# Optimization experiments

Measured on AMD Instinct MI355X. Metric: run time of the kernel, lower is better.

The kernel has to match this reference:

```python
import jax, jax.numpy as jnp
import numpy as np

N_NODES = 100000
N_EDGES = 3200000
IN_FEAT = 512
HID = 32
N_CLASSES = 10


def gcn_conv(x, W, b, src, dst, num_nodes):
    """PyG GCNConv: linear transform, then symmetric-normalized aggregation
    with self-loops. out_i = sum_{j->i} norm_ij * (x_j W) + d_i^{-1} * (x_i W) + b."""
    h = x @ W  # [N, out]
    ones = jnp.ones(src.shape[0], dtype=x.dtype)
    deg = jax.ops.segment_sum(ones, dst, num_segments=num_nodes) + 1.0  # +1 self-loop
    dinv = jax.lax.rsqrt(deg)
    norm = dinv[src] * dinv[dst]  # [E]
    msg = h[src] * norm[:, None]  # [E, out]
    agg = jax.ops.segment_sum(msg, dst, num_segments=num_nodes)
    agg = agg + h * (dinv * dinv)[:, None]  # self-loop term (norm = d^-1)
    return agg + b


def setup_inputs() -> dict:
    key = jax.random.key(0)
    ks = jax.random.split(key, 12)
    x0 = jax.random.normal(ks[0], (N_NODES, IN_FEAT), dtype=jnp.float32)
    edge_index = jax.random.randint(ks[1], (2, N_EDGES), 0, N_NODES, dtype=jnp.int64)
    batch = jnp.zeros((N_NODES,), dtype=jnp.int64)

    def glorot(k, shape):
        fan_in, fan_out = shape
        lim = jnp.sqrt(6.0 / (fan_in + fan_out)).astype(jnp.float32)
        return jax.random.uniform(k, shape, jnp.float32, -lim, lim)

    return {
        "x0": x0,
        "edge_index": edge_index,
        "batch": batch,
        "W1": glorot(ks[2], (IN_FEAT, HID)),
        "b1": jnp.zeros((HID,), jnp.float32),
        "W2": glorot(ks[3], (HID, HID)),
        "b2": jnp.zeros((HID,), jnp.float32),
        "W3": glorot(ks[4], (HID, HID)),
        "b3": jnp.zeros((HID,), jnp.float32),
        "lin1_W": glorot(ks[5], (HID, 16)),
        "lin1_b": jnp.zeros((16,), jnp.float32),
        "lin2_W": glorot(ks[6], (16, N_CLASSES)),
        "lin2_b": jnp.zeros((N_CLASSES,), jnp.float32),
    }


def reference(x0, edge_index, batch, W1, b1, W2, b2, W3, b3,
              lin1_W, lin1_b, lin2_W, lin2_b):
    src, dst = edge_index[0], edge_index[1]
    n = x0.shape[0]
    x1 = jax.nn.relu(gcn_conv(x0, W1, b1, src, dst, n))
    x2 = jax.nn.relu(gcn_conv(x1, W2, b2, src, dst, n))
    x3 = jax.nn.relu(gcn_conv(x2, W3, b3, src, dst, n))
    # NOTE: original code computes cat([x1,x2,x3]) but then uses only x3; we match that.
    x = jax.nn.relu(x3 @ lin1_W + lin1_b)
    # dropout p=0.5 is identity in eval mode
    x = x @ lin2_W + lin2_b
    return x
```

## Files before the change

kernel.cpp:

```cpp
#include <hip/hip_runtime.h>
#include <hip/hip_bf16.h>

typedef float f32x4 __attribute__((ext_vector_type(4)));

#define N_NODES 100000
#define NCHUNK 16

__global__ void k_detect(const int* __restrict__ ei, int* __restrict__ mode) {
    __shared__ int flag;
    if (threadIdx.x == 0) flag = 0;
    __syncthreads();
    int f = 0;
    for (int i = threadIdx.x; i < 4096; i += 256)
        if (ei[2 * i + 1] != 0) f = 1;
    if (f) flag = 1;
    __syncthreads();
    if (threadIdx.x == 0) *mode = flag;
}

__global__ void k_zero(int* p, int n) {
    int i = blockIdx.x * 256 + threadIdx.x;
    if (i < n) p[i] = 0;
}

__global__ void k_pack_hist(const int* __restrict__ ei, const int* __restrict__ mode,
                            int2* __restrict__ pairs, int* __restrict__ cnt, int E) {
    int e = blockIdx.x * 256 + threadIdx.x;
    if (e >= E) return;
    int m = *mode;
    int s = m ? ei[e] : ei[2 * e];
    int d = m ? ei[E + e] : ei[2 * (E + e)];
    if ((unsigned)s >= N_NODES) s = 0;
    if ((unsigned)d >= N_NODES) d = 0;
    int2 p; p.x = s; p.y = d;
    pairs[e] = p;
    atomicAdd(&cnt[d], 1);
}

__global__ void k_bsum(const int* __restrict__ cnt, int* __restrict__ bsum, int n) {
    __shared__ int s[256];
    int tid = threadIdx.x;
    int i = blockIdx.x * 256 + tid;
    s[tid] = (i < n) ? cnt[i] : 0;
    __syncthreads();
    for (int d = 128; d > 0; d >>= 1) {
        if (tid < d) s[tid] += s[tid + d];
        __syncthreads();
    }
    if (tid == 0) bsum[blockIdx.x] = s[0];
}

__global__ void k_scan_top(const int* __restrict__ bsum, int* __restrict__ boff, int nb) {
    __shared__ int s[512];
    int tid = threadIdx.x;
    int v = (tid < nb) ? bsum[tid] : 0;
    s[tid] = v;
    __syncthreads();
    for (int d = 1; d < 512; d <<= 1) {
        int t = (tid >= d) ? s[tid - d] : 0;
        __syncthreads();
        s[tid] += t;
        __syncthreads();
    }
    if (tid < nb) boff[tid] = s[tid] - v;
}

__global__ void k_scan_bot(const int* __restrict__ cnt, const int* __restrict__ boff,
                           int* __restrict__ rowptr, float* __restrict__ dinv,
                           int* __restrict__ fill, int n) {
    __shared__ int s[256];
    int tid = threadIdx.x;
    int i = blockIdx.x * 256 + tid;
    int v = (i < n) ? cnt[i] : 0;
    s[tid] = v;
    __syncthreads();
    for (int d = 1; d < 256; d <<= 1) {
        int t = (tid >= d) ? s[tid - d] : 0;
        __syncthreads();
        s[tid] += t;
        __syncthreads();
    }
    int incl = s[tid];
    if (i < n) {
        rowptr[i] = boff[blockIdx.x] + incl - v;
        if (i == n - 1) rowptr[n] = boff[blockIdx.x] + incl;
        dinv[i] = rsqrtf((float)v + 1.0f);
        fill[i] = 0;
    }
}

__global__ __launch_bounds__(256) void k_scatter(const int4* __restrict__ pairs4,
                                                 const int* __restrict__ rowptr,
                                                 int* __restrict__ fill,
                                                 int* __restrict__ csr, int half) {
    int gtid = blockIdx.x * 256 + threadIdx.x;
    int gstride = gridDim.x * 256;
    const int CH = (N_NODES + NCHUNK - 1) / NCHUNK;
    for (int c = 0; c < NCHUNK; c++) {
        int lo = c * CH;
        for (int i = gtid; i < half; i += gstride) {
            int4 p = pairs4[i];
            if ((unsigned)(p.y - lo) < (unsigned)CH) {
                int pos = rowptr[p.y] + atomicAdd(&fill[p.y], 1);
                csr[pos] = p.x;
            }
            if ((unsigned)(p.w - lo) < (unsigned)CH) {
                int pos = rowptr[p.w] + atomicAdd(&fill[p.w], 1);
                csr[pos] = p.z;
            }
        }
    }
}

__global__ __launch_bounds__(256) void k_gemm1(const float* __restrict__ X,
                                               const float* __restrict__ W,
                                               float* __restrict__ H) {
    __shared__ float lds[8448];
    float* xs  = lds;
    float* wsw = lds + 4160;
    int tid = threadIdx.x;
    int row = tid & 63;
    int kc  = tid >> 6;
    long row0 = (long)blockIdx.x * 64;

    float acc[32];
#pragma unroll
    for (int c = 0; c < 32; c++) acc[c] = 0.f;

    for (int k0 = 0; k0 < 512; k0 += 64) {
        __syncthreads();
#pragma unroll
        for (int u = 0; u < 8; u++) {
            int idx = u * 256 + tid;
            wsw[idx] = W[k0 * 32 + idx];
        }
#pragma unroll
        for (int u = 0; u < 4; u++) {
            int idx = u * 256 + tid;
            int rr = idx >> 4, j = idx & 15;
            long grow = row0 + rr;
            f32x4 v = {0.f, 0.f, 0.f, 0.f};
            if (grow < N_NODES) v = *(const f32x4*)&X[grow * 512 + k0 + 4 * j];
            float* dp = &xs[rr * 65 + 4 * j];
            dp[0] = v.x; dp[1] = v.y; dp[2] = v.z; dp[3] = v.w;
        }
        __syncthreads();
        int kbase = kc * 16;
#pragma unroll
        for (int kk = 0; kk < 16; kk++) {
            float xk = xs[row * 65 + kbase + kk];
            const float* wrow = &wsw[(kbase + kk) * 32];
#pragma unroll
            for (int c = 0; c < 32; c += 4) {
                f32x4 wv = *(const f32x4*)&wrow[c];
                acc[c]     += xk * wv.x;
                acc[c + 1] += xk * wv.y;
                acc[c + 2] += xk * wv.z;
                acc[c + 3] += xk * wv.w;
            }
        }
    }
    __syncthreads();
#pragma unroll
    for (int c = 0; c < 32; c++) lds[(kc * 64 + row) * 33 + c] = acc[c];
    __syncthreads();
#pragma unroll
    for (int i = 0; i < 8; i++) {
        int o = i * 256 + tid;
        int r = o >> 5, c = o & 31;
        float s = lds[r * 33 + c] + lds[(64 + r) * 33 + c]
                + lds[(128 + r) * 33 + c] + lds[(192 + r) * 33 + c];
        long grow = row0 + r;
        if (grow < N_NODES) H[grow * 32 + c] = s;
    }
}

__global__ __launch_bounds__(256) void k_agg_mm(const float* __restrict__ H,
                                                const int* __restrict__ rowptr,
                                                const int* __restrict__ csr,
                                                const float* __restrict__ dinv,
                                                const float* __restrict__ bias,
                                                const float* __restrict__ W,
                                                float* __restrict__ Hout, int n) {
    __shared__ float ws[1024];
    int tid = threadIdx.x;
    for (int t = tid; t < 1024; t += 256) ws[t] = W[t];
    __syncthreads();
    int node = blockIdx.x * 8 + (tid >> 5);
    int f = tid & 31;
    if (node >= n) return;
    int e0 = rowptr[node], e1 = rowptr[node + 1];
    float a0 = 0.f, a1 = 0.f, a2 = 0.f, a3 = 0.f;
    int e = e0;
    for (; e + 3 < e1; e += 4) {
        int s0 = csr[e], s1 = csr[e + 1], s2 = csr[e + 2], s3 = csr[e + 3];
        a0 += H[(long)s0 * 32 + f] * dinv[s0];
        a1 += H[(long)s1 * 32 + f] * dinv[s1];
        a2 += H[(long)s2 * 32 + f] * dinv[s2];
        a3 += H[(long)s3 * 32 + f] * dinv[s3];
    }
    for (; e < e1; e++) {
        int s0 = csr[e];
        a0 += H[(long)s0 * 32 + f] * dinv[s0];
    }
    float dv = dinv[node];
    float v = ((a0 + a1) + (a2 + a3)) * dv + H[(long)node * 32 + f] * dv * dv + bias[f];
    v = fmaxf(v, 0.f);
    float o = 0.f;
#pragma unroll
    for (int k = 0; k < 32; k++) {
        float vk = __shfl(v, k, 32);
        o += vk * ws[k * 32 + f];
    }
    Hout[(long)node * 32 + f] = o;
}

__global__ __launch_bounds__(256) void k_agg_head(const float* __restrict__ H,
                                                  const int* __restrict__ rowptr,
                                                  const int* __restrict__ csr,
                                                  const float* __restrict__ dinv,
                                                  const float* __restrict__ bias,
                                                  const float* __restrict__ L1W,
                                                  const float* __restrict__ L1B,
                                                  const float* __restrict__ L2W,
                                                  const float* __restrict__ L2B,
                                                  float* __restrict__ out, int n) {
    __shared__ float w1[512];
    __shared__ float w2[160];
    __shared__ float bb1[16];
    __shared__ float bb2[10];
    int tid = threadIdx.x;
    for (int t = tid; t < 512; t += 256) w1[t] = L1W[t];
    if (tid < 160) w2[tid] = L2W[tid];
    if (tid < 16) bb1[tid] = L1B[tid];
    if (tid < 10) bb2[tid] = L2B[tid];
    __syncthreads();
    int node = blockIdx.x * 8 + (tid >> 5);
    int f = tid & 31;
    if (node >= n) return;
    int e0 = rowptr[node], e1 = rowptr[node + 1];
    float a0 = 0.f, a1 = 0.f, a2 = 0.f, a3 = 0.f;
    int e = e0;
    for (; e + 3 < e1; e += 4) {
        int s0 = csr[e], s1 = csr[e + 1], s2 = csr[e + 2], s3 = csr[e + 3];
        a0 += H[(long)s0 * 32 + f] * dinv[s0];
        a1 += H[(long)s1 * 32 + f] * dinv[s1];
        a2 += H[(long)s2 * 32 + f] * dinv[s2];
        a3 += H[(long)s3 * 32 + f] * dinv[s3];
    }
    for (; e < e1; e++) {
        int s0 = csr[e];
        a0 += H[(long)s0 * 32 + f] * dinv[s0];
    }
    float dv = dinv[node];
    float v = ((a0 + a1) + (a2 + a3)) * dv + H[(long)node * 32 + f] * dv * dv + bias[f];
    v = fmaxf(v, 0.f);
    int c1 = f & 15;
    float t1 = 0.f;
#pragma unroll
    for (int k = 0; k < 32; k++) {
        float vk = __shfl(v, k, 32);
        t1 += vk * w1[k * 16 + c1];
    }
    t1 = fmaxf(t1 + bb1[c1], 0.f);
    int c2 = (f < 10) ? f : 0;
    float o = 0.f;
#pragma unroll
    for (int k = 0; k < 16; k++) {
        float tk = __shfl(t1, k, 32);
        o += tk * w2[k * 10 + c2];
    }
    o += bb2[c2];
    if (f < 10) out[(long)node * 10 + f] = o;
}

extern "C" void kernel_launch(void* const* d_in, const int* in_sizes, int n_in,
                              void* d_out, int out_size, void* d_ws, size_t ws_size,
                              hipStream_t stream) {
    const float* x0 = (const float*)d_in[0];
    const int* ei = (const int*)d_in[1];
    const float* W1 = (const float*)d_in[3];
    const float* b1 = (const float*)d_in[4];
    const float* W2 = (const float*)d_in[5];
    const float* b2 = (const float*)d_in[6];
    const float* W3 = (const float*)d_in[7];
    const float* b3 = (const float*)d_in[8];
    const float* l1W = (const float*)d_in[9];
    const float* l1b = (const float*)d_in[10];
    const float* l2W = (const float*)d_in[11];
    const float* l2b = (const float*)d_in[12];

    const int E = in_sizes[1] / 2;
    const int N = N_NODES;

    char* w = (char*)d_ws;
    float* h      = (float*)(w);
    float* xb     = (float*)(w + 12800000);
    int2*  pairs  = (int2*) (w);
    int*   cnt    = (int*)  (w + 25600000);
    int*   rowptr = (int*)  (w + 26000000);
    float* dinv   = (float*)(w + 26400016);
    int*   fill   = (int*)  (w + 26800016);
    int*   bsum   = (int*)  (w + 27200016);
    int*   boff   = (int*)  (w + 27204016);
    int*   csr    = (int*)  (w + 27208016);
    int*   mode   = (int*)  (w + 40008016);

    const int NB  = (N + 255) / 256;
    const int EB  = (E + 255) / 256;
    const int AGB = (N + 7) / 8;
    const int G1B = (N + 63) / 64;

    k_detect<<<1, 256, 0, stream>>>(ei, mode);
    k_zero<<<NB, 256, 0, stream>>>(cnt, N);
    k_pack_hist<<<EB, 256, 0, stream>>>(ei, mode, pairs, cnt, E);
    k_bsum<<<NB, 256, 0, stream>>>(cnt, bsum, N);
    k_scan_top<<<1, 512, 0, stream>>>(bsum, boff, NB);
    k_scan_bot<<<NB, 256, 0, stream>>>(cnt, boff, rowptr, dinv, fill, N);
    k_scatter<<<1024, 256, 0, stream>>>((const int4*)pairs, rowptr, fill, csr, E / 2);

    k_gemm1<<<G1B, 256, 0, stream>>>(x0, W1, h);
    k_agg_mm<<<AGB, 256, 0, stream>>>(h, rowptr, csr, dinv, b1, W2, xb, N);
    k_agg_mm<<<AGB, 256, 0, stream>>>(xb, rowptr, csr, dinv, b2, W3, h, N);
    k_agg_head<<<AGB, 256, 0, stream>>>(h, rowptr, csr, dinv, b3,
                                        l1W, l1b, l2W, l2b, (float*)d_out, N);
}
```

Measured before the change: 924.3 us.

## Build CSR via two-level bucket sort and pre-scale features by dinv

Replaces the global-atomic histogram and the chunked 16-pass scatter with a two-level counting sort. Per-block LDS histograms over 256-node buckets feed column scans, edges are bucketized, then each bucket builds its CSR slice with LDS atomics. Source features are pre-multiplied by dinv in the GEMM and aggregation epilogues, which removes the per-edge dinv gather. The gather loop now loads 32 neighbor indices cooperatively and broadcasts them with shuffles. In exchange it adds more kernel launches and an intermediate bucketed pair buffer, and it reorders the floating-point summation.

```diff
diff --git a/kernel.cpp b/kernel.cpp
--- a/kernel.cpp
+++ b/kernel.cpp
@@ -4,7 +4,9 @@
 typedef float f32x4 __attribute__((ext_vector_type(4)));
 
 #define N_NODES 100000
-#define NCHUNK 16
+#define NBUK 391
+#define BSHIFT 8
+#define HBLK 256
 
 __global__ void k_detect(const int* __restrict__ ei, int* __restrict__ mode) {
     __shared__ int flag;
@@ -18,42 +20,41 @@
     if (threadIdx.x == 0) *mode = flag;
 }
 
-__global__ void k_zero(int* p, int n) {
-    int i = blockIdx.x * 256 + threadIdx.x;
-    if (i < n) p[i] = 0;
-}
-
-__global__ void k_pack_hist(const int* __restrict__ ei, const int* __restrict__ mode,
-                            int2* __restrict__ pairs, int* __restrict__ cnt, int E) {
-    int e = blockIdx.x * 256 + threadIdx.x;
-    if (e >= E) return;
+__global__ __launch_bounds__(256) void k_hist(const int* __restrict__ ei,
+                                              const int* __restrict__ mode,
+                                              int* __restrict__ gh, int E, int chunk) {
+    __shared__ int hist[NBUK];
+    int tid = threadIdx.x, k = blockIdx.x;
+    for (int b = tid; b < NBUK; b += 256) hist[b] = 0;
+    __syncthreads();
     int m = *mode;
-    int s = m ? ei[e] : ei[2 * e];
-    int d = m ? ei[E + e] : ei[2 * (E + e)];
-    if ((unsigned)s >= N_NODES) s = 0;
-    if ((unsigned)d >= N_NODES) d = 0;
-    int2 p; p.x = s; p.y = d;
-    pairs[e] = p;
-    atomicAdd(&cnt[d], 1);
-}
-
-__global__ void k_bsum(const int* __restrict__ cnt, int* __restrict__ bsum, int n) {
+    int e0 = k * chunk, e1 = min(E, e0 + chunk);
+    for (int e = e0 + tid; e < e1; e += 256) {
+        int d = m ? ei[E + e] : ei[2 * (E + e)];
+        if ((unsigned)d >= N_NODES) d = 0;
+        atomicAdd(&hist[d >> BSHIFT], 1);
+    }
+    __syncthreads();
+    for (int b = tid; b < NBUK; b += 256) gh[k * NBUK + b] = hist[b];
+}
+
+__global__ __launch_bounds__(256) void k_btot(const int* __restrict__ gh, int* __restrict__ btot) {
     __shared__ int s[256];
-    int tid = threadIdx.x;
-    int i = blockIdx.x * 256 + tid;
-    s[tid] = (i < n) ? cnt[i] : 0;
+    int b = blockIdx.x, tid = threadIdx.x;
+    s[tid] = gh[tid * NBUK + b];
     __syncthreads();
     for (int d = 128; d > 0; d >>= 1) {
         if (tid < d) s[tid] += s[tid + d];
         __syncthreads();
     }
-    if (tid == 0) bsum[blockIdx.x] = s[0];
-}
-
-__global__ void k_scan_top(const int* __restrict__ bsum, int* __restrict__ boff, int nb) {
+    if (tid == 0) btot[b] = s[0];
+}
+
+__global__ void k_scan_btot(const int* __restrict__ btot, int* __restrict__ bbase,
+                            int* __restrict__ rowptr, int E) {
     __shared__ int s[512];
     int tid = threadIdx.x;
-    int v = (tid < nb) ? bsum[tid] : 0;
+    int v = (tid < NBUK) ? btot[tid] : 0;
     s[tid] = v;
     __syncthreads();
     for (int d = 1; d < 512; d <<= 1) {
@@ -62,16 +63,14 @@
         s[tid] += t;
         __syncthreads();
     }
-    if (tid < nb) boff[tid] = s[tid] - v;
-}
-
-__global__ void k_scan_bot(const int* __restrict__ cnt, const int* __restrict__ boff,
-                           int* __restrict__ rowptr, float* __restrict__ dinv,
-                           int* __restrict__ fill, int n) {
+    if (tid < NBUK) bbase[tid] = s[tid] - v;
+    if (tid == 0) { bbase[NBUK] = E; rowptr[N_NODES] = E; }
+}
+
+__global__ __launch_bounds__(256) void k_scan_cols(int* __restrict__ gh, const int* __restrict__ bbase) {
     __shared__ int s[256];
-    int tid = threadIdx.x;
-    int i = blockIdx.x * 256 + tid;
-    int v = (i < n) ? cnt[i] : 0;
+    int b = blockIdx.x, tid = threadIdx.x;
+    int v = gh[tid * NBUK + b];
     s[tid] = v;
     __syncthreads();
     for (int d = 1; d < 256; d <<= 1) {
@@ -80,40 +79,76 @@
         s[tid] += t;
         __syncthreads();
     }
-    int incl = s[tid];
-    if (i < n) {
-        rowptr[i] = boff[blockIdx.x] + incl - v;
-        if (i == n - 1) rowptr[n] = boff[blockIdx.x] + incl;
-        dinv[i] = rsqrtf((float)v + 1.0f);
-        fill[i] = 0;
-    }
-}
-
-__global__ __launch_bounds__(256) void k_scatter(const int4* __restrict__ pairs4,
-                                                 const int* __restrict__ rowptr,
-                                                 int* __restrict__ fill,
-                                                 int* __restrict__ csr, int half) {
-    int gtid = blockIdx.x * 256 + threadIdx.x;
-    int gstride = gridDim.x * 256;
-    const int CH = (N_NODES + NCHUNK - 1) / NCHUNK;
-    for (int c = 0; c < NCHUNK; c++) {
-        int lo = c * CH;
-        for (int i = gtid; i < half; i += gstride) {
-            int4 p = pairs4[i];
-            if ((unsigned)(p.y - lo) < (unsigned)CH) {
-                int pos = rowptr[p.y] + atomicAdd(&fill[p.y], 1);
-                csr[pos] = p.x;
-            }
-            if ((unsigned)(p.w - lo) < (unsigned)CH) {
-                int pos = rowptr[p.w] + atomicAdd(&fill[p.w], 1);
-                csr[pos] = p.z;
-            }
-        }
+    gh[tid * NBUK + b] = bbase[b] + s[tid] - v;
+}
+
+__global__ __launch_bounds__(256) void k_bucketize(const int* __restrict__ ei,
+                                                   const int* __restrict__ mode,
+                                                   const int* __restrict__ offs,
+                                                   int2* __restrict__ bp, int E, int chunk) {
+    __shared__ int cur[NBUK];
+    int tid = threadIdx.x, k = blockIdx.x;
+    for (int b = tid; b < NBUK; b += 256) cur[b] = offs[k * NBUK + b];
+    __syncthreads();
+    int m = *mode;
+    int e0 = k * chunk, e1 = min(E, e0 + chunk);
+    for (int e = e0 + tid; e < e1; e += 256) {
+        int s, d;
+        if (m) { s = ei[e]; d = ei[E + e]; }
+        else   { s = ei[2 * e]; d = ei[2 * (E + e)]; }
+        if ((unsigned)s >= N_NODES) s = 0;
+        if ((unsigned)d >= N_NODES) d = 0;
+        int pos = atomicAdd(&cur[d >> BSHIFT], 1);
+        int2 p; p.x = s; p.y = d;
+        bp[pos] = p;
+    }
+}
+
+__global__ __launch_bounds__(256) void k_build_csr(const int2* __restrict__ bp,
+                                                   const int* __restrict__ bbase,
+                                                   int* __restrict__ rowptr,
+                                                   float* __restrict__ dinv,
+                                                   int* __restrict__ csr) {
+    __shared__ int cnt[256];
+    __shared__ int s[256];
+    __shared__ int cur[256];
+    int b = blockIdx.x, tid = threadIdx.x;
+    int nb = b << BSHIFT;
+    int estart = bbase[b], eend = bbase[b + 1];
+    cnt[tid] = 0;
+    __syncthreads();
+    for (int e = estart + tid; e < eend; e += 256) {
+        int2 p = bp[e];
+        atomicAdd(&cnt[p.y - nb], 1);
+    }
+    __syncthreads();
+    int v = cnt[tid];
+    s[tid] = v;
+    __syncthreads();
+    for (int d = 1; d < 256; d <<= 1) {
+        int t = (tid >= d) ? s[tid - d] : 0;
+        __syncthreads();
+        s[tid] += t;
+        __syncthreads();
+    }
+    int excl = s[tid] - v;
+    int node = nb + tid;
+    if (node < N_NODES) {
+        rowptr[node] = estart + excl;
+        dinv[node] = rsqrtf((float)v + 1.0f);
+    }
+    cur[tid] = estart + excl;
+    __syncthreads();
+    for (int e = estart + tid; e < eend; e += 256) {
+        int2 p = bp[e];
+        int pos = atomicAdd(&cur[p.y - nb], 1);
+        csr[pos] = p.x;
     }
 }
 
 __global__ __launch_bounds__(256) void k_gemm1(const float* __restrict__ X,
                                                const float* __restrict__ W,
+                                               const float* __restrict__ dinv,
                                                float* __restrict__ H) {
     __shared__ float lds[8448];
     float* xs  = lds;
@@ -168,11 +203,41 @@
     for (int i = 0; i < 8; i++) {
         int o = i * 256 + tid;
         int r = o >> 5, c = o & 31;
-        float s = lds[r * 33 + c] + lds[(64 + r) * 33 + c]
-                + lds[(128 + r) * 33 + c] + lds[(192 + r) * 33 + c];
+        float sv = lds[r * 33 + c] + lds[(64 + r) * 33 + c]
+                 + lds[(128 + r) * 33 + c] + lds[(192 + r) * 33 + c];
         long grow = row0 + r;
-        if (grow < N_NODES) H[grow * 32 + c] = s;
-    }
+        if (grow < N_NODES) H[grow * 32 + c] = sv * dinv[grow];
+    }
+}
+
+__device__ __forceinline__ float gather_sum(const float* __restrict__ Hf,
+                                            const int* __restrict__ csr,
+                                            int e0, int e1, int f) {
+    float a0 = 0.f, a1 = 0.f, a2 = 0.f, a3 = 0.f;
+    for (int base = e0; base < e1; base += 32) {
+        int idx = base + f;
+        int sl = (idx < e1) ? csr[idx] : 0;
+        int mm = e1 - base;
+        if (mm >= 32) {
+#pragma unroll
+            for (int j = 0; j < 32; j += 4) {
+                int s0 = __shfl(sl, j, 32);
+                int s1 = __shfl(sl, j + 1, 32);
+                int s2 = __shfl(sl, j + 2, 32);
+                int s3 = __shfl(sl, j + 3, 32);
+                a0 += Hf[(long)s0 * 32];
+                a1 += Hf[(long)s1 * 32];
+                a2 += Hf[(long)s2 * 32];
+                a3 += Hf[(long)s3 * 32];
+            }
+        } else {
+            for (int j = 0; j < mm; j++) {
+                int s0 = __shfl(sl, j, 32);
+                a0 += Hf[(long)s0 * 32];
+            }
+        }
+    }
+    return (a0 + a1) + (a2 + a3);
 }
 
 __global__ __launch_bounds__(256) void k_agg_mm(const float* __restrict__ H,
@@ -190,21 +255,10 @@
     int f = tid & 31;
     if (node >= n) return;
     int e0 = rowptr[node], e1 = rowptr[node + 1];
-    float a0 = 0.f, a1 = 0.f, a2 = 0.f, a3 = 0.f;
-    int e = e0;
-    for (; e + 3 < e1; e += 4) {
-        int s0 = csr[e], s1 = csr[e + 1], s2 = csr[e + 2], s3 = csr[e + 3];
-        a0 += H[(long)s0 * 32 + f] * dinv[s0];
-        a1 += H[(long)s1 * 32 + f] * dinv[s1];
-        a2 += H[(long)s2 * 32 + f] * dinv[s2];
-        a3 += H[(long)s3 * 32 + f] * dinv[s3];
-    }
-    for (; e < e1; e++) {
-        int s0 = csr[e];
-        a0 += H[(long)s0 * 32 + f] * dinv[s0];
-    }
+    const float* Hf = H + f;
+    float asum = gather_sum(Hf, csr, e0, e1, f);
     float dv = dinv[node];
-    float v = ((a0 + a1) + (a2 + a3)) * dv + H[(long)node * 32 + f] * dv * dv + bias[f];
+    float v = dv * (asum + Hf[(long)node * 32]) + bias[f];
     v = fmaxf(v, 0.f);
     float o = 0.f;
 #pragma unroll
@@ -212,7 +266,7 @@
         float vk = __shfl(v, k, 32);
         o += vk * ws[k * 32 + f];
     }
-    Hout[(long)node * 32 + f] = o;
+    Hout[(long)node * 32 + f] = o * dv;
 }
 
 __global__ __launch_bounds__(256) void k_agg_head(const float* __restrict__ H,
@@ -239,21 +293,10 @@
     int f = tid & 31;
     if (node >= n) return;
     int e0 = rowptr[node], e1 = rowptr[node + 1];
-    float a0 = 0.f, a1 = 0.f, a2 = 0.f, a3 = 0.f;
-    int e = e0;
-    for (; e + 3 < e1; e += 4) {
-        int s0 = csr[e], s1 = csr[e + 1], s2 = csr[e + 2], s3 = csr[e + 3];
-        a0 += H[(long)s0 * 32 + f] * dinv[s0];
-        a1 += H[(long)s1 * 32 + f] * dinv[s1];
-        a2 += H[(long)s2 * 32 + f] * dinv[s2];
-        a3 += H[(long)s3 * 32 + f] * dinv[s3];
-    }
-    for (; e < e1; e++) {
-        int s0 = csr[e];
-        a0 += H[(long)s0 * 32 + f] * dinv[s0];
-    }
+    const float* Hf = H + f;
+    float asum = gather_sum(Hf, csr, e0, e1, f);
     float dv = dinv[node];
-    float v = ((a0 + a1) + (a2 + a3)) * dv + H[(long)node * 32 + f] * dv * dv + bias[f];
+    float v = dv * (asum + Hf[(long)node * 32]) + bias[f];
     v = fmaxf(v, 0.f);
     int c1 = f & 15;
     float t1 = 0.f;
@@ -296,30 +339,28 @@
     char* w = (char*)d_ws;
     float* h      = (float*)(w);
     float* xb     = (float*)(w + 12800000);
-    int2*  pairs  = (int2*) (w);
-    int*   cnt    = (int*)  (w + 25600000);
-    int*   rowptr = (int*)  (w + 26000000);
-    float* dinv   = (float*)(w + 26400016);
-    int*   fill   = (int*)  (w + 26800016);
-    int*   bsum   = (int*)  (w + 27200016);
-    int*   boff   = (int*)  (w + 27204016);
-    int*   csr    = (int*)  (w + 27208016);
-    int*   mode   = (int*)  (w + 40008016);
-
-    const int NB  = (N + 255) / 256;
-    const int EB  = (E + 255) / 256;
+    int2*  bp     = (int2*) (w);
+    int*   gh     = (int*)  (w + 25600000);
+    int*   btot   = (int*)  (w + 26000384);
+    int*   bbase  = (int*)  (w + 26001948);
+    int*   rowptr = (int*)  (w + 26003516);
+    float* dinv   = (float*)(w + 26403532);
+    int*   csr    = (int*)  (w + 26803532);
+    int*   mode   = (int*)  (w + 39603532);
+
+    const int chunk = (E + HBLK - 1) / HBLK;
     const int AGB = (N + 7) / 8;
     const int G1B = (N + 63) / 64;
 
     k_detect<<<1, 256, 0, stream>>>(ei, mode);
-    k_zero<<<NB, 256, 0, stream>>>(cnt, N);
-    k_pack_hist<<<EB, 256, 0, stream>>>(ei, mode, pairs, cnt, E);
-    k_bsum<<<NB, 256, 0, stream>>>(cnt, bsum, N);
-    k_scan_top<<<1, 512, 0, stream>>>(bsum, boff, NB);
-    k_scan_bot<<<NB, 256, 0, stream>>>(cnt, boff, rowptr, dinv, fill, N);
-    k_scatter<<<1024, 256, 0, stream>>>((const int4*)pairs, rowptr, fill, csr, E / 2);
-
-    k_gemm1<<<G1B, 256, 0, stream>>>(x0, W1, h);
+    k_hist<<<HBLK, 256, 0, stream>>>(ei, mode, gh, E, chunk);
+    k_btot<<<NBUK, 256, 0, stream>>>(gh, btot);
+    k_scan_btot<<<1, 512, 0, stream>>>(btot, bbase, rowptr, E);
+    k_scan_cols<<<NBUK, 256, 0, stream>>>(gh, bbase);
+    k_bucketize<<<HBLK, 256, 0, stream>>>(ei, mode, gh, bp, E, chunk);
+    k_build_csr<<<NBUK, 256, 0, stream>>>(bp, bbase, rowptr, dinv, csr);
+
+    k_gemm1<<<G1B, 256, 0, stream>>>(x0, W1, dinv, h);
     k_agg_mm<<<AGB, 256, 0, stream>>>(h, rowptr, csr, dinv, b1, W2, xb, N);
     k_agg_mm<<<AGB, 256, 0, stream>>>(xb, rowptr, csr, dinv, b2, W3, h, N);
     k_agg_head<<<AGB, 256, 0, stream>>>(h, rowptr, csr, dinv, b3,
```

After: 792.7 us. -14.2%, faster.
